# Kernel tuning notes

Hardware: AMD Instinct MI355X
Metric: run time of the kernel (lower is better)

## Reference

```python
import jax, jax.numpy as jnp
import numpy as np

B, S, D = 2, 2048, 1024
M = 2048          # d_mlp
E = 8             # num_experts
TOP_K = 2


def setup_inputs() -> dict:
    key = jax.random.key(0)
    ks = jax.random.split(key, 5)
    std = 0.02
    return {
        "residual": jax.random.normal(ks[0], (B, S, D), jnp.float32),
        "W_router": jax.random.normal(ks[1], (D, E), jnp.float32) * std,
        "W_gate": jax.random.normal(ks[2], (E, D, M), jnp.float32) * std,
        "b_gate": jnp.zeros((E, M), jnp.float32),
        "W_up": jax.random.normal(ks[3], (E, D, M), jnp.float32) * std,
        "b_up": jnp.zeros((E, M), jnp.float32),
        "W_out": jax.random.normal(ks[4], (E, M, D), jnp.float32) * std,
        "b_out": jnp.zeros((E, D), jnp.float32),
    }


def reference(residual, W_router, W_gate, b_gate, W_up, b_up, W_out, b_out):
    # --- router: softmax over experts, top-k selection, renormalize ---
    router_logits = jnp.einsum('bsd,de->bse', residual, W_router)
    router_probs = jax.nn.softmax(router_logits, axis=-1)
    top_k_probs, top_k_idx = jax.lax.top_k(router_probs, TOP_K)          # [B,S,K]
    top_k_probs = top_k_probs / (jnp.sum(top_k_probs, -1, keepdims=True) + 1e-8)
    # per-expert combine weight [B,S,E]; top-k indices are unique per token
    one_hot = jax.nn.one_hot(top_k_idx, E, dtype=residual.dtype)          # [B,S,K,E]
    expert_weights = jnp.einsum('bsk,bske->bse', top_k_probs, one_hot)
    # --- each expert runs dense SwiGLU MLP on the FULL batch (compute-then-mask, as in source) ---
    gate = jax.nn.silu(jnp.einsum('bsd,edm->ebsm', residual, W_gate) + b_gate[:, None, None, :])
    up = jnp.einsum('bsd,edm->ebsm', residual, W_up) + b_up[:, None, None, :]
    hidden = gate * up                                                    # [E,B,S,M]
    expert_out = jnp.einsum('ebsm,emd->ebsd', hidden, W_out) + b_out[:, None, None, :]
    # --- weighted combine (weights are zero for non-selected experts) ---
    output = jnp.einsum('bse,ebsd->bsd', expert_weights, expert_out)
    return output
```

## Files before the change

kernel.cpp:

```cpp
#include <hip/hip_runtime.h>
#include <cstdint>
#include <cstddef>

#define TT 4096
#define DD 1024
#define MM 2048
#define EE 8
#define NPAIR 8192

typedef unsigned short u16;
typedef __bf16 bf16x8 __attribute__((ext_vector_type(8)));
typedef float f32x4 __attribute__((ext_vector_type(4)));
typedef u16 u16x8 __attribute__((ext_vector_type(8)));
typedef __attribute__((address_space(3))) void* lds_vp;
typedef __attribute__((address_space(1))) const void* gbl_cvp;

__device__ __forceinline__ void async16(u16* l, const u16* g) {
  __builtin_amdgcn_global_load_lds((gbl_cvp)(const void*)g, (lds_vp)(void*)l, 16, 0, 0);
}

#define VMCNT6() asm volatile("s_waitcnt vmcnt(6)" ::: "memory")
#define VMCNT4() asm volatile("s_waitcnt vmcnt(4)" ::: "memory")
#define VMCNT0() asm volatile("s_waitcnt vmcnt(0)" ::: "memory")
#define BARR() do { asm volatile("" ::: "memory"); __builtin_amdgcn_s_barrier(); asm volatile("" ::: "memory"); } while (0)

__device__ __forceinline__ u16 f2bf(float f) {
  uint32_t u = __builtin_bit_cast(uint32_t, f);
  u += 0x7fffu + ((u >> 16) & 1u);
  return (u16)(u >> 16);
}
__device__ __forceinline__ float bf2f(u16 h) {
  uint32_t u = ((uint32_t)h) << 16;
  return __builtin_bit_cast(float, u);
}

__global__ void router_kernel(const float* __restrict__ X, const float* __restrict__ Wr,
                              int* __restrict__ tok_idx, float* __restrict__ wpair,
                              u16* __restrict__ Xbf) {
  int wave = threadIdx.x >> 6;
  int lane = threadIdx.x & 63;
  int t = blockIdx.x * 4 + wave;
  const float4* x4 = (const float4*)(X + (size_t)t * DD);
  float acc[EE];
#pragma unroll
  for (int e = 0; e < EE; e++) acc[e] = 0.f;
#pragma unroll
  for (int i = 0; i < 4; i++) {
    float4 xv = x4[i * 64 + lane];
    ushort4 o;
    o.x = f2bf(xv.x); o.y = f2bf(xv.y); o.z = f2bf(xv.z); o.w = f2bf(xv.w);
    *(ushort4*)&Xbf[(size_t)t * DD + (size_t)(i * 64 + lane) * 4] = o;
    const float4* wr4 = (const float4*)(Wr + (size_t)(i * 256 + lane * 4) * EE);
    float xs[4] = {xv.x, xv.y, xv.z, xv.w};
#pragma unroll
    for (int c = 0; c < 4; c++) {
      float4 wa = wr4[c * 2 + 0];
      float4 wb = wr4[c * 2 + 1];
      acc[0] += xs[c] * wa.x; acc[1] += xs[c] * wa.y;
      acc[2] += xs[c] * wa.z; acc[3] += xs[c] * wa.w;
      acc[4] += xs[c] * wb.x; acc[5] += xs[c] * wb.y;
      acc[6] += xs[c] * wb.z; acc[7] += xs[c] * wb.w;
    }
  }
#pragma unroll
  for (int off = 32; off > 0; off >>= 1)
#pragma unroll
    for (int e = 0; e < EE; e++) acc[e] += __shfl_xor(acc[e], off);
  if (lane == 0) {
    float mx = acc[0];
#pragma unroll
    for (int e = 1; e < EE; e++) mx = fmaxf(mx, acc[e]);
    float p[EE], s = 0.f;
#pragma unroll
    for (int e = 0; e < EE; e++) { p[e] = __expf(acc[e] - mx); s += p[e]; }
    float inv = 1.f / s;
#pragma unroll
    for (int e = 0; e < EE; e++) p[e] *= inv;
    int i0 = 0;
#pragma unroll
    for (int e = 1; e < EE; e++) if (p[e] > p[i0]) i0 = e;
    int i1 = (i0 == 0) ? 1 : 0;
#pragma unroll
    for (int e = 0; e < EE; e++) if (e != i0 && p[e] > p[i1]) i1 = e;
    float denom = p[i0] + p[i1] + 1e-8f;
    tok_idx[t * 2 + 0] = i0;
    tok_idx[t * 2 + 1] = i1;
    wpair[t * 2 + 0] = p[i0] / denom;
    wpair[t * 2 + 1] = p[i1] / denom;
  }
}

__global__ void bucket_kernel(const int* __restrict__ tok_idx, int* __restrict__ offsets,
                              int* __restrict__ bucket) {
  __shared__ int lcnt[EE];
  __shared__ int lcur[EE];
  int tid = threadIdx.x;
  int lane = tid & 63;
  if (tid < EE) lcnt[tid] = 0;
  __syncthreads();
  {
    int cnt[EE];
#pragma unroll
    for (int k = 0; k < EE; k++) cnt[k] = 0;
    for (int i = tid; i < NPAIR; i += 1024) {
      int e = tok_idx[i];
#pragma unroll
      for (int k = 0; k < EE; k++) {
        unsigned long long m = __ballot(e == k);
        cnt[k] += __popcll(m);
      }
    }
    if (lane == 0) {
#pragma unroll
      for (int k = 0; k < EE; k++)
        if (cnt[k]) atomicAdd(&lcnt[k], cnt[k]);
    }
  }
  __syncthreads();
  if (tid == 0) {
    int s = 0;
    for (int e = 0; e < EE; e++) {
      offsets[e] = s;
      lcur[e] = s;
      s += lcnt[e];
    }
    offsets[EE] = s;
  }
  __syncthreads();
  for (int i = tid; i < NPAIR; i += 1024) {
    int e = tok_idx[i];
    int pos = 0;
#pragma unroll
    for (int k = 0; k < EE; k++) {
      unsigned long long m = __ballot(e == k);
      int c = __popcll(m);
      if (c) {
        int leader = (int)__ffsll((long long)m) - 1;
        int base = 0;
        if (lane == leader) base = atomicAdd(&lcur[k], c);
        base = __shfl(base, leader);
        if (e == k) pos = base + __popcll(m & ((1ull << lane) - 1ull));
      }
    }
    bucket[pos] = i;
  }
}

__global__ __launch_bounds__(256)
void transpose_cvt(const float* __restrict__ in, u16* __restrict__ out, int R, int C) {
  __shared__ float tile[64][65];
  int e = blockIdx.z;
  const float* I = in + (size_t)e * R * C;
  u16* O = out + (size_t)e * R * C;
  int c0 = blockIdx.x * 64, r0 = blockIdx.y * 64;
  int t = threadIdx.x;
  {
    int cq = t & 15;
    int rb = t >> 4;
#pragma unroll
    for (int i = 0; i < 4; i++) {
      int r = rb + i * 16;
      float4 v = *(const float4*)&I[(size_t)(r0 + r) * C + c0 + cq * 4];
      tile[cq * 4 + 0][r] = v.x;
      tile[cq * 4 + 1][r] = v.y;
      tile[cq * 4 + 2][r] = v.z;
      tile[cq * 4 + 3][r] = v.w;
    }
  }
  __syncthreads();
  {
    int rseg = (t & 7) * 8;
    int cc = t >> 3;
#pragma unroll
    for (int i = 0; i < 2; i++) {
      int c = cc + i * 32;
      u16x8 o;
#pragma unroll
      for (int k = 0; k < 8; k++) o[k] = f2bf(tile[c][rseg + k]);
      *(u16x8*)&O[(size_t)(c0 + c) * R + r0 + rseg] = o;
    }
  }
}

__device__ __forceinline__ bool tile_map(const int* __restrict__ offsets, int x,
                                         int& expert, int& row0, int& rows) {
  expert = -1;
#pragma unroll 1
  for (int e = 0; e < EE; e++) {
    int o0 = offsets[e], o1 = offsets[e + 1];
    int nt = (o1 - o0 + 127) >> 7;
    if (x < nt) { expert = e; row0 = o0 + (x << 7); rows = min(128, o1 - row0); return true; }
    x -= nt;
  }
  return false;
}

template <int NTLOG2>
__device__ __forceinline__ void grid_decode(int bid, int& rt, int& n0) {
  int xcd = bid & 7, slot = bid >> 3;
  rt = xcd * 9 + (slot >> NTLOG2);
  n0 = (slot & ((1 << NTLOG2) - 1)) * 128;
}


__global__ __launch_bounds__(256, 2)
void moe_gemm_gu(const u16* __restrict__ Xbf, const u16* __restrict__ WtG,
                 const u16* __restrict__ WtU, const float* __restrict__ bgate,
                 const float* __restrict__ bup, u16* __restrict__ Hws,
                 const int* __restrict__ offsets, const int* __restrict__ bucket) {
  int rt, n0;
  grid_decode<4>(blockIdx.x, rt, n0);
  int expert, row0, rows;
  if (!tile_map(offsets, rt, expert, row0, rows)) return;

  __shared__ u16 Alds[3 * 128 * 32];
  __shared__ u16 Glds[3 * 128 * 32];
  __shared__ u16 Ulds[3 * 128 * 32];

  int tid = threadIdx.x;
  int wave = tid >> 6, lane = tid & 63;
  int wm = wave >> 1, wn = wave & 1;
  int quad = lane >> 4, l15 = lane & 15;
  int swz = ((lane & 3) ^ ((lane >> 3) & 3)) * 8;
  int rp  = (quad ^ ((l15 >> 1) & 3)) * 8;

  long arow0, arow1;
  {
    int r0l = wave * 32 + (lane >> 2);
    int rr0 = min(r0l, rows - 1);
    int rr1 = min(r0l + 16, rows - 1);
    arow0 = (long)(bucket[row0 + rr0] >> 1) * DD;
    arow1 = (long)(bucket[row0 + rr1] >> 1) * DD;
  }
  const u16* A0 = Xbf + arow0 + swz;
  const u16* A1 = Xbf + arow1 + swz;
  size_t bo = (size_t)expert * MM * DD + (size_t)n0 * DD
            + (long)(wave * 32 + (lane >> 2)) * DD + swz;
  const u16* G0 = WtG + bo; const u16* G1 = G0 + 16 * DD;
  const u16* U0 = WtU + bo; const u16* U1 = U0 + 16 * DD;

  int sb0 = (wave * 32) * 32, sb1 = (wave * 32 + 16) * 32;

  f32x4 accG[4][4], accU[4][4];
#pragma unroll
  for (int i = 0; i < 4; i++)
#pragma unroll
    for (int j = 0; j < 4; j++) { accG[i][j] = (f32x4){0,0,0,0}; accU[i][j] = (f32x4){0,0,0,0}; }

  auto stage = [&](int b) {
    int bo2 = b * (128 * 32);
    async16(&Alds[bo2 + sb0], A0); async16(&Alds[bo2 + sb1], A1);
    async16(&Glds[bo2 + sb0], G0); async16(&Glds[bo2 + sb1], G1);
    async16(&Ulds[bo2 + sb0], U0); async16(&Ulds[bo2 + sb1], U1);
    A0 += 32; A1 += 32; G0 += 32; G1 += 32; U0 += 32; U1 += 32;
  };

  auto compute = [&](int b) {
    int ro = b * (128 * 32);
    bf16x8 af[4], bf[4];
#pragma unroll
    for (int i = 0; i < 4; i++) {
      af[i] = *(const bf16x8*)&Alds[ro + (wm * 64 + i * 16 + l15) * 32 + rp];
      bf[i] = *(const bf16x8*)&Glds[ro + (wn * 64 + i * 16 + l15) * 32 + rp];
    }
    __builtin_amdgcn_s_setprio(1);
#pragma unroll
    for (int i = 0; i < 4; i++)
#pragma unroll
      for (int j = 0; j < 4; j++)
        accG[i][j] = __builtin_amdgcn_mfma_f32_16x16x32_bf16(af[i], bf[j], accG[i][j], 0, 0, 0);
    __builtin_amdgcn_s_setprio(0);
#pragma unroll
    for (int i = 0; i < 4; i++)
      bf[i] = *(const bf16x8*)&Ulds[ro + (wn * 64 + i * 16 + l15) * 32 + rp];
    __builtin_amdgcn_s_setprio(1);
#pragma unroll
    for (int i = 0; i < 4; i++)
#pragma unroll
      for (int j = 0; j < 4; j++)
        accU[i][j] = __builtin_amdgcn_mfma_f32_16x16x32_bf16(af[i], bf[j], accU[i][j], 0, 0, 0);
    __builtin_amdgcn_s_setprio(0);
  };

  constexpr int NT = DD / 32;
  stage(0);
  stage(1);
  int br = 0, bs = 2;
#pragma unroll 1
  for (int t = 0; t < NT - 2; ++t) {
    VMCNT6();
    BARR();
    stage(bs);
    compute(br);
    bs = br; br = (br + 1 == 3) ? 0 : br + 1;
  }
  VMCNT6(); BARR(); compute(br); br = (br + 1 == 3) ? 0 : br + 1;
  VMCNT0(); BARR(); compute(br);

#pragma unroll
  for (int i = 0; i < 4; i++) {
    int lrb = wm * 64 + i * 16 + quad * 4;
#pragma unroll
    for (int j = 0; j < 4; j++) {
      int gc = n0 + wn * 64 + j * 16 + l15;
      float bg = bgate[expert * MM + gc];
      float bu = bup[expert * MM + gc];
#pragma unroll
      for (int r = 0; r < 4; r++) {
        int lr = lrb + r;
        if (lr < rows) {
          int grow = row0 + lr;
          float g = accG[i][j][r] + bg;
          float u = accU[i][j][r] + bu;
          float sg = g / (1.f + __expf(-g));
          Hws[(size_t)grow * MM + gc] = f2bf(sg * u);
        }
      }
    }
  }
}

__global__ __launch_bounds__(256, 3)
void moe_gemm_out(const u16* __restrict__ Hmat, const u16* __restrict__ WtO,
                  const float* __restrict__ bias, float* __restrict__ Ypart,
                  const int* __restrict__ offsets, const int* __restrict__ bucket,
                  const float* __restrict__ wpair) {
  int rt, n0;
  grid_decode<3>(blockIdx.x, rt, n0);
  int expert, row0, rows;
  if (!tile_map(offsets, rt, expert, row0, rows)) return;

  __shared__ u16 Alds[3 * 128 * 32];
  __shared__ u16 Blds[3 * 128 * 32];

  int tid = threadIdx.x;
  int wave = tid >> 6, lane = tid & 63;
  int wm = wave >> 1, wn = wave & 1;
  int quad = lane >> 4, l15 = lane & 15;
  int swz = ((lane & 3) ^ ((lane >> 3) & 3)) * 8;
  int rp  = (quad ^ ((l15 >> 1) & 3)) * 8;

  long arow0, arow1;
  {
    int r0l = wave * 32 + (lane >> 2);
    int rr0 = min(r0l, rows - 1);
    int rr1 = min(r0l + 16, rows - 1);
    arow0 = (long)(row0 + rr0) * MM;
    arow1 = (long)(row0 + rr1) * MM;
  }
  const u16* A0 = Hmat + arow0 + swz;
  const u16* A1 = Hmat + arow1 + swz;
  const u16* B0 = WtO + (size_t)expert * DD * MM + (size_t)n0 * MM
                + (long)(wave * 32 + (lane >> 2)) * MM + swz;
  const u16* B1 = B0 + 16 * MM;

  int sb0 = (wave * 32) * 32, sb1 = (wave * 32 + 16) * 32;

  f32x4 acc[4][4];
#pragma unroll
  for (int i = 0; i < 4; i++)
#pragma unroll
    for (int j = 0; j < 4; j++) acc[i][j] = (f32x4){0, 0, 0, 0};

  auto stage = [&](int b) {
    int bo2 = b * (128 * 32);
    async16(&Alds[bo2 + sb0], A0); async16(&Alds[bo2 + sb1], A1);
    async16(&Blds[bo2 + sb0], B0); async16(&Blds[bo2 + sb1], B1);
    A0 += 32; A1 += 32; B0 += 32; B1 += 32;
  };

  auto compute = [&](int b) {
    int ro = b * (128 * 32);
    bf16x8 af[4], bf[4];
#pragma unroll
    for (int i = 0; i < 4; i++) {
      af[i] = *(const bf16x8*)&Alds[ro + (wm * 64 + i * 16 + l15) * 32 + rp];
      bf[i] = *(const bf16x8*)&Blds[ro + (wn * 64 + i * 16 + l15) * 32 + rp];
    }
    __builtin_amdgcn_s_setprio(1);
#pragma unroll
    for (int i = 0; i < 4; i++)
#pragma unroll
      for (int j = 0; j < 4; j++)
        acc[i][j] = __builtin_amdgcn_mfma_f32_16x16x32_bf16(af[i], bf[j], acc[i][j], 0, 0, 0);
    __builtin_amdgcn_s_setprio(0);
  };

  constexpr int NT = MM / 32;
  stage(0);
  stage(1);
  int br = 0, bs = 2;
#pragma unroll 1
  for (int t = 0; t < NT - 2; ++t) {
    VMCNT4();
    BARR();
    stage(bs);
    compute(br);
    bs = br; br = (br + 1 == 3) ? 0 : br + 1;
  }
  VMCNT4(); BARR(); compute(br); br = (br + 1 == 3) ? 0 : br + 1;
  VMCNT0(); BARR(); compute(br);

#pragma unroll
  for (int i = 0; i < 4; i++) {
    int lrb = wm * 64 + i * 16 + quad * 4;
#pragma unroll
    for (int j = 0; j < 4; j++) {
      int gc = n0 + wn * 64 + j * 16 + l15;
      float bv = bias[expert * DD + gc];
#pragma unroll
      for (int r = 0; r < 4; r++) {
        int lr = lrb + r;
        if (lr < rows) {
          int grow = row0 + lr;
          int p = bucket[grow];
          float w = wpair[p];
          Ypart[(size_t)p * DD + gc] = w * (acc[i][j][r] + bv);
        }
      }
    }
  }
}

__global__ void combine_kernel(const float* __restrict__ Ypart, float* __restrict__ out) {
  int i = blockIdx.x * 256 + threadIdx.x;
  int t = i >> 8;
  int c4 = i & 255;
  const float4* y0 = (const float4*)(Ypart + (size_t)(2 * t) * DD) + c4;
  const float4* y1 = (const float4*)(Ypart + (size_t)(2 * t + 1) * DD) + c4;
  float4 a = *y0, b = *y1;
  float4 o;
  o.x = a.x + b.x; o.y = a.y + b.y; o.z = a.z + b.z; o.w = a.w + b.w;
  ((float4*)out)[i] = o;
}

extern "C" void kernel_launch(void* const* d_in, const int* in_sizes, int n_in,
                              void* d_out, int out_size, void* d_ws, size_t ws_size,
                              hipStream_t stream) {
  const float* residual = (const float*)d_in[0];
  const float* W_router = (const float*)d_in[1];
  const float* W_gate   = (const float*)d_in[2];
  const float* b_gate   = (const float*)d_in[3];
  const float* W_up     = (const float*)d_in[4];
  const float* b_up     = (const float*)d_in[5];
  const float* W_out    = (const float*)d_in[6];
  const float* b_out    = (const float*)d_in[7];
  float* out = (float*)d_out;

  char* ws = (char*)d_ws;
  int*   tok_idx = (int*)(ws + 0);
  float* wpair   = (float*)(ws + 32768);
  int*   offsets = (int*)(ws + 65536);
  int*   bucket  = (int*)(ws + 65536 + 512);
  u16*   Xbf  = (u16*)(ws + 131072);
  u16*   WtG  = Xbf + (size_t)TT * DD;
  u16*   WtU  = WtG + (size_t)EE * MM * DD;
  u16*   WtO  = WtU + (size_t)EE * MM * DD;
  u16*   Hws  = WtO + (size_t)EE * DD * MM;
  float* Ypart = (float*)(Hws + (size_t)NPAIR * MM);

  router_kernel<<<dim3(TT / 4), dim3(256), 0, stream>>>(residual, W_router, tok_idx, wpair, Xbf);
  bucket_kernel<<<dim3(1), dim3(1024), 0, stream>>>(tok_idx, offsets, bucket);
  transpose_cvt<<<dim3(MM / 64, DD / 64, EE), dim3(256), 0, stream>>>(W_gate, WtG, DD, MM);
  transpose_cvt<<<dim3(MM / 64, DD / 64, EE), dim3(256), 0, stream>>>(W_up,   WtU, DD, MM);
  transpose_cvt<<<dim3(DD / 64, MM / 64, EE), dim3(256), 0, stream>>>(W_out,  WtO, MM, DD);
  moe_gemm_gu<<<dim3(8 * 9 * 16), dim3(256), 0, stream>>>(Xbf, WtG, WtU, b_gate, b_up, Hws, offsets, bucket);
  moe_gemm_out<<<dim3(8 * 9 * 8), dim3(256), 0, stream>>>(Hws, WtO, b_out, Ypart, offsets, bucket, wpair);
  combine_kernel<<<dim3(TT * DD / 4 / 256), dim3(256), 0, stream>>>(Ypart, out);
}
```

Measured before the change: 468.0 us.

## Fuse router and weight transposes into one prep kernel, retune GEMM scheduling

Merges the router kernel and the three weight transpose/convert launches into a single prep kernel that dispatches on block index, cutting launch overhead and letting the two kinds of work overlap. It also changes grid decoding so consecutive slots within an XCD walk row tiles before column tiles, which is meant to improve weight reuse in L2. The gate/up GEMM now loads both B fragments up front and issues all MFMAs under one priority window, and the main loops are partially unrolled. The cost is higher register pressure in the GEMMs and a larger, more branchy prep kernel.

```diff
diff --git a/kernel.cpp b/kernel.cpp
--- a/kernel.cpp
+++ b/kernel.cpp
@@ -34,59 +34,107 @@
   return __builtin_bit_cast(float, u);
 }
 
-__global__ void router_kernel(const float* __restrict__ X, const float* __restrict__ Wr,
-                              int* __restrict__ tok_idx, float* __restrict__ wpair,
-                              u16* __restrict__ Xbf) {
-  int wave = threadIdx.x >> 6;
-  int lane = threadIdx.x & 63;
-  int t = blockIdx.x * 4 + wave;
-  const float4* x4 = (const float4*)(X + (size_t)t * DD);
-  float acc[EE];
-#pragma unroll
-  for (int e = 0; e < EE; e++) acc[e] = 0.f;
-#pragma unroll
-  for (int i = 0; i < 4; i++) {
-    float4 xv = x4[i * 64 + lane];
-    ushort4 o;
-    o.x = f2bf(xv.x); o.y = f2bf(xv.y); o.z = f2bf(xv.z); o.w = f2bf(xv.w);
-    *(ushort4*)&Xbf[(size_t)t * DD + (size_t)(i * 64 + lane) * 4] = o;
-    const float4* wr4 = (const float4*)(Wr + (size_t)(i * 256 + lane * 4) * EE);
-    float xs[4] = {xv.x, xv.y, xv.z, xv.w};
-#pragma unroll
-    for (int c = 0; c < 4; c++) {
-      float4 wa = wr4[c * 2 + 0];
-      float4 wb = wr4[c * 2 + 1];
-      acc[0] += xs[c] * wa.x; acc[1] += xs[c] * wa.y;
-      acc[2] += xs[c] * wa.z; acc[3] += xs[c] * wa.w;
-      acc[4] += xs[c] * wb.x; acc[5] += xs[c] * wb.y;
-      acc[6] += xs[c] * wb.z; acc[7] += xs[c] * wb.w;
-    }
-  }
-#pragma unroll
-  for (int off = 32; off > 0; off >>= 1)
-#pragma unroll
-    for (int e = 0; e < EE; e++) acc[e] += __shfl_xor(acc[e], off);
-  if (lane == 0) {
-    float mx = acc[0];
-#pragma unroll
-    for (int e = 1; e < EE; e++) mx = fmaxf(mx, acc[e]);
-    float p[EE], s = 0.f;
-#pragma unroll
-    for (int e = 0; e < EE; e++) { p[e] = __expf(acc[e] - mx); s += p[e]; }
-    float inv = 1.f / s;
-#pragma unroll
-    for (int e = 0; e < EE; e++) p[e] *= inv;
-    int i0 = 0;
-#pragma unroll
-    for (int e = 1; e < EE; e++) if (p[e] > p[i0]) i0 = e;
-    int i1 = (i0 == 0) ? 1 : 0;
-#pragma unroll
-    for (int e = 0; e < EE; e++) if (e != i0 && p[e] > p[i1]) i1 = e;
-    float denom = p[i0] + p[i1] + 1e-8f;
-    tok_idx[t * 2 + 0] = i0;
-    tok_idx[t * 2 + 1] = i1;
-    wpair[t * 2 + 0] = p[i0] / denom;
-    wpair[t * 2 + 1] = p[i1] / denom;
+__global__ __launch_bounds__(256)
+void prep_kernel(const float* __restrict__ X, const float* __restrict__ Wr,
+                 int* __restrict__ tok_idx, float* __restrict__ wpair,
+                 u16* __restrict__ Xbf,
+                 const float* __restrict__ Gf, const float* __restrict__ Uf,
+                 const float* __restrict__ Of, u16* __restrict__ tG,
+                 u16* __restrict__ tU, u16* __restrict__ tO) {
+  __shared__ float tile[64][65];
+  int bid = blockIdx.x;
+  if (bid < TT / 4) {
+    int wave = threadIdx.x >> 6;
+    int lane = threadIdx.x & 63;
+    int t = bid * 4 + wave;
+    const float4* x4 = (const float4*)(X + (size_t)t * DD);
+    float acc[EE];
+#pragma unroll
+    for (int e = 0; e < EE; e++) acc[e] = 0.f;
+#pragma unroll
+    for (int i = 0; i < 4; i++) {
+      float4 xv = x4[i * 64 + lane];
+      ushort4 o;
+      o.x = f2bf(xv.x); o.y = f2bf(xv.y); o.z = f2bf(xv.z); o.w = f2bf(xv.w);
+      *(ushort4*)&Xbf[(size_t)t * DD + (size_t)(i * 64 + lane) * 4] = o;
+      const float4* wr4 = (const float4*)(Wr + (size_t)(i * 256 + lane * 4) * EE);
+      float xs[4] = {xv.x, xv.y, xv.z, xv.w};
+#pragma unroll
+      for (int c = 0; c < 4; c++) {
+        float4 wa = wr4[c * 2 + 0];
+        float4 wb = wr4[c * 2 + 1];
+        acc[0] += xs[c] * wa.x; acc[1] += xs[c] * wa.y;
+        acc[2] += xs[c] * wa.z; acc[3] += xs[c] * wa.w;
+        acc[4] += xs[c] * wb.x; acc[5] += xs[c] * wb.y;
+        acc[6] += xs[c] * wb.z; acc[7] += xs[c] * wb.w;
+      }
+    }
+#pragma unroll
+    for (int off = 32; off > 0; off >>= 1)
+#pragma unroll
+      for (int e = 0; e < EE; e++) acc[e] += __shfl_xor(acc[e], off);
+    if (lane == 0) {
+      float mx = acc[0];
+#pragma unroll
+      for (int e = 1; e < EE; e++) mx = fmaxf(mx, acc[e]);
+      float p[EE], s = 0.f;
+#pragma unroll
+      for (int e = 0; e < EE; e++) { p[e] = __expf(acc[e] - mx); s += p[e]; }
+      float inv = 1.f / s;
+#pragma unroll
+      for (int e = 0; e < EE; e++) p[e] *= inv;
+      int i0 = 0;
+#pragma unroll
+      for (int e = 1; e < EE; e++) if (p[e] > p[i0]) i0 = e;
+      int i1 = (i0 == 0) ? 1 : 0;
+#pragma unroll
+      for (int e = 0; e < EE; e++) if (e != i0 && p[e] > p[i1]) i1 = e;
+      float denom = p[i0] + p[i1] + 1e-8f;
+      tok_idx[t * 2 + 0] = i0;
+      tok_idx[t * 2 + 1] = i1;
+      wpair[t * 2 + 0] = p[i0] / denom;
+      wpair[t * 2 + 1] = p[i1] / denom;
+    }
+    return;
+  }
+  int idx = bid - TT / 4;
+  int z = idx >> 9;
+  int tidx = idx & 511;
+  const float* in; u16* out; int R, C, shift, e;
+  if (z < 8)       { in = Gf; out = tG; R = DD; C = MM; e = z;      shift = 5; }
+  else if (z < 16) { in = Uf; out = tU; R = DD; C = MM; e = z - 8;  shift = 5; }
+  else             { in = Of; out = tO; R = MM; C = DD; e = z - 16; shift = 4; }
+  int cx = tidx & ((1 << shift) - 1);
+  int cy = tidx >> shift;
+  const float* I = in + (size_t)e * R * C;
+  u16* O = out + (size_t)e * R * C;
+  int c0 = cx * 64, r0 = cy * 64;
+  int t = threadIdx.x;
+  {
+    int cq = t & 15;
+    int rb = t >> 4;
+#pragma unroll
+    for (int i = 0; i < 4; i++) {
+      int r = rb + i * 16;
+      float4 v = *(const float4*)&I[(size_t)(r0 + r) * C + c0 + cq * 4];
+      tile[cq * 4 + 0][r] = v.x;
+      tile[cq * 4 + 1][r] = v.y;
+      tile[cq * 4 + 2][r] = v.z;
+      tile[cq * 4 + 3][r] = v.w;
+    }
+  }
+  __syncthreads();
+  {
+    int rseg = (t & 7) * 8;
+    int cc = t >> 3;
+#pragma unroll
+    for (int i = 0; i < 2; i++) {
+      int c = cc + i * 32;
+      u16x8 o;
+#pragma unroll
+      for (int k = 0; k < 8; k++) o[k] = f2bf(tile[c][rseg + k]);
+      *(u16x8*)&O[(size_t)(c0 + c) * R + r0 + rseg] = o;
+    }
   }
 }
 
@@ -146,42 +194,6 @@
   }
 }
 
-__global__ __launch_bounds__(256)
-void transpose_cvt(const float* __restrict__ in, u16* __restrict__ out, int R, int C) {
-  __shared__ float tile[64][65];
-  int e = blockIdx.z;
-  const float* I = in + (size_t)e * R * C;
-  u16* O = out + (size_t)e * R * C;
-  int c0 = blockIdx.x * 64, r0 = blockIdx.y * 64;
-  int t = threadIdx.x;
-  {
-    int cq = t & 15;
-    int rb = t >> 4;
-#pragma unroll
-    for (int i = 0; i < 4; i++) {
-      int r = rb + i * 16;
-      float4 v = *(const float4*)&I[(size_t)(r0 + r) * C + c0 + cq * 4];
-      tile[cq * 4 + 0][r] = v.x;
-      tile[cq * 4 + 1][r] = v.y;
-      tile[cq * 4 + 2][r] = v.z;
-      tile[cq * 4 + 3][r] = v.w;
-    }
-  }
-  __syncthreads();
-  {
-    int rseg = (t & 7) * 8;
-    int cc = t >> 3;
-#pragma unroll
-    for (int i = 0; i < 2; i++) {
-      int c = cc + i * 32;
-      u16x8 o;
-#pragma unroll
-      for (int k = 0; k < 8; k++) o[k] = f2bf(tile[c][rseg + k]);
-      *(u16x8*)&O[(size_t)(c0 + c) * R + r0 + rseg] = o;
-    }
-  }
-}
-
 __device__ __forceinline__ bool tile_map(const int* __restrict__ offsets, int x,
                                          int& expert, int& row0, int& rows) {
   expert = -1;
@@ -195,11 +207,10 @@
   return false;
 }
 
-template <int NTLOG2>
 __device__ __forceinline__ void grid_decode(int bid, int& rt, int& n0) {
   int xcd = bid & 7, slot = bid >> 3;
-  rt = xcd * 9 + (slot >> NTLOG2);
-  n0 = (slot & ((1 << NTLOG2) - 1)) * 128;
+  rt = xcd * 9 + slot % 9;
+  n0 = (slot / 9) * 128;
 }
 
 
@@ -209,7 +220,7 @@
                  const float* __restrict__ bup, u16* __restrict__ Hws,
                  const int* __restrict__ offsets, const int* __restrict__ bucket) {
   int rt, n0;
-  grid_decode<4>(blockIdx.x, rt, n0);
+  grid_decode(blockIdx.x, rt, n0);
   int expert, row0, rows;
   if (!tile_map(offsets, rt, expert, row0, rows)) return;
 
@@ -257,28 +268,24 @@
 
   auto compute = [&](int b) {
     int ro = b * (128 * 32);
-    bf16x8 af[4], bf[4];
+    bf16x8 af[4], bg[4], bu[4];
 #pragma unroll
     for (int i = 0; i < 4; i++) {
       af[i] = *(const bf16x8*)&Alds[ro + (wm * 64 + i * 16 + l15) * 32 + rp];
-      bf[i] = *(const bf16x8*)&Glds[ro + (wn * 64 + i * 16 + l15) * 32 + rp];
+      bg[i] = *(const bf16x8*)&Glds[ro + (wn * 64 + i * 16 + l15) * 32 + rp];
+      bu[i] = *(const bf16x8*)&Ulds[ro + (wn * 64 + i * 16 + l15) * 32 + rp];
     }
     __builtin_amdgcn_s_setprio(1);
 #pragma unroll
     for (int i = 0; i < 4; i++)
 #pragma unroll
       for (int j = 0; j < 4; j++)
-        accG[i][j] = __builtin_amdgcn_mfma_f32_16x16x32_bf16(af[i], bf[j], accG[i][j], 0, 0, 0);
-    __builtin_amdgcn_s_setprio(0);
+        accG[i][j] = __builtin_amdgcn_mfma_f32_16x16x32_bf16(af[i], bg[j], accG[i][j], 0, 0, 0);
 #pragma unroll
     for (int i = 0; i < 4; i++)
-      bf[i] = *(const bf16x8*)&Ulds[ro + (wn * 64 + i * 16 + l15) * 32 + rp];
-    __builtin_amdgcn_s_setprio(1);
-#pragma unroll
-    for (int i = 0; i < 4; i++)
 #pragma unroll
       for (int j = 0; j < 4; j++)
-        accU[i][j] = __builtin_amdgcn_mfma_f32_16x16x32_bf16(af[i], bf[j], accU[i][j], 0, 0, 0);
+        accU[i][j] = __builtin_amdgcn_mfma_f32_16x16x32_bf16(af[i], bu[j], accU[i][j], 0, 0, 0);
     __builtin_amdgcn_s_setprio(0);
   };
 
@@ -286,7 +293,7 @@
   stage(0);
   stage(1);
   int br = 0, bs = 2;
-#pragma unroll 1
+#pragma unroll 3
   for (int t = 0; t < NT - 2; ++t) {
     VMCNT6();
     BARR();
@@ -303,15 +310,15 @@
 #pragma unroll
     for (int j = 0; j < 4; j++) {
       int gc = n0 + wn * 64 + j * 16 + l15;
-      float bg = bgate[expert * MM + gc];
-      float bu = bup[expert * MM + gc];
+      float bgv = bgate[expert * MM + gc];
+      float buv = bup[expert * MM + gc];
 #pragma unroll
       for (int r = 0; r < 4; r++) {
         int lr = lrb + r;
         if (lr < rows) {
           int grow = row0 + lr;
-          float g = accG[i][j][r] + bg;
-          float u = accU[i][j][r] + bu;
+          float g = accG[i][j][r] + bgv;
+          float u = accU[i][j][r] + buv;
           float sg = g / (1.f + __expf(-g));
           Hws[(size_t)grow * MM + gc] = f2bf(sg * u);
         }
@@ -326,7 +333,7 @@
                   const int* __restrict__ offsets, const int* __restrict__ bucket,
                   const float* __restrict__ wpair) {
   int rt, n0;
-  grid_decode<3>(blockIdx.x, rt, n0);
+  grid_decode(blockIdx.x, rt, n0);
   int expert, row0, rows;
   if (!tile_map(offsets, rt, expert, row0, rows)) return;
 
@@ -390,7 +397,7 @@
   stage(0);
   stage(1);
   int br = 0, bs = 2;
-#pragma unroll 1
+#pragma unroll 2
   for (int t = 0; t < NT - 2; ++t) {
     VMCNT4();
     BARR();
@@ -459,11 +466,9 @@
   u16*   Hws  = WtO + (size_t)EE * DD * MM;
   float* Ypart = (float*)(Hws + (size_t)NPAIR * MM);
 
-  router_kernel<<<dim3(TT / 4), dim3(256), 0, stream>>>(residual, W_router, tok_idx, wpair, Xbf);
+  prep_kernel<<<dim3(TT / 4 + 24 * 512), dim3(256), 0, stream>>>(
+      residual, W_router, tok_idx, wpair, Xbf, W_gate, W_up, W_out, WtG, WtU, WtO);
   bucket_kernel<<<dim3(1), dim3(1024), 0, stream>>>(tok_idx, offsets, bucket);
-  transpose_cvt<<<dim3(MM / 64, DD / 64, EE), dim3(256), 0, stream>>>(W_gate, WtG, DD, MM);
-  transpose_cvt<<<dim3(MM / 64, DD / 64, EE), dim3(256), 0, stream>>>(W_up,   WtU, DD, MM);
-  transpose_cvt<<<dim3(DD / 64, MM / 64, EE), dim3(256), 0, stream>>>(W_out,  WtO, MM, DD);
   moe_gemm_gu<<<dim3(8 * 9 * 16), dim3(256), 0, stream>>>(Xbf, WtG, WtU, b_gate, b_up, Hws, offsets, bucket);
   moe_gemm_out<<<dim3(8 * 9 * 8), dim3(256), 0, stream>>>(Hws, WtO, b_out, Ypart, offsets, bucket, wpair);
   combine_kernel<<<dim3(TT * DD / 4 / 256), dim3(256), 0, stream>>>(Ypart, out);
```

Result: faster. 447.0 us (-4.5%).
